# Kernel tuning notes

Measured on AMD Instinct MI355X. Metric: run time of the kernel, lower is better.

Reference implementation:

```python
import jax, jax.numpy as jnp
import numpy as np
from jax import lax

BS, EN, SEQ = 512, 512, 64
D_ENT, D_IN, D_KEY, D_F, H = 256, 1024, 32, 256, 32


def _layer_norm(x, g, b, eps=1e-5):
    m = x.mean(-1, keepdims=True)
    v = ((x - m) ** 2).mean(-1, keepdims=True)
    return (x - m) * lax.rsqrt(v + eps) * g + b


def setup_inputs() -> dict:
    key = jax.random.key(0)
    ks = jax.random.split(key, 24)
    f32 = jnp.float32

    def w(k, shape, fan_in):
        return (jax.random.normal(k, shape, dtype=f32) / np.sqrt(fan_in)).astype(f32)

    inp = {
        'entity_embedding': jax.random.normal(ks[0], (BS, EN, D_ENT), dtype=f32),
        'autoregressive_embedding': jax.random.normal(ks[1], (BS, D_IN), dtype=f32),
        'entity_num': jax.random.randint(ks[2], (BS,), 0, EN),
        'selected_units': jax.random.randint(ks[3], (BS, SEQ), 0, EN),
        'selected_units_num': jax.random.randint(ks[4], (BS,), 0, SEQ),
        # fc_block params (Linear: y = x @ W + b)
        'key_fc_w': w(ks[5], (D_ENT, D_KEY), D_ENT), 'key_fc_b': jnp.zeros((D_KEY,), f32),
        'q1_w': w(ks[6], (D_IN, D_F), D_IN), 'q1_b': jnp.zeros((D_F,), f32),
        'q2_w': w(ks[7], (D_F, D_KEY), D_F), 'q2_b': jnp.zeros((D_KEY,), f32),
        'e1_w': w(ks[8], (D_KEY, D_F), D_KEY), 'e1_b': jnp.zeros((D_F,), f32),
        'e2_w': w(ks[9], (D_F, D_IN), D_F), 'e2_b': jnp.zeros((D_IN,), f32),
        'end_embedding': jax.random.uniform(ks[10], (D_KEY,), dtype=f32,
                                            minval=-1.0 / np.sqrt(D_KEY), maxval=1.0 / np.sqrt(D_KEY)),
        # LayerNorm-LSTM (single layer), gate order: i, f, g, o
        'w_ih': w(ks[11], (D_KEY, 4 * H), D_KEY),
        'w_hh': w(ks[12], (H, 4 * H), H),
        'ln_ig': 1.0 + 0.1 * jax.random.normal(ks[13], (4 * H,), dtype=f32),
        'ln_ib': 0.1 * jax.random.normal(ks[14], (4 * H,), dtype=f32),
        'ln_hg': 1.0 + 0.1 * jax.random.normal(ks[15], (4 * H,), dtype=f32),
        'ln_hb': 0.1 * jax.random.normal(ks[16], (4 * H,), dtype=f32),
        'ln_cg': 1.0 + 0.1 * jax.random.normal(ks[17], (H,), dtype=f32),
        'ln_cb': 0.1 * jax.random.normal(ks[18], (H,), dtype=f32),
    }
    return inp


def _forward(entity_embedding, autoregressive_embedding, entity_num, selected_units,
             selected_units_num, key_fc_w, key_fc_b, q1_w, q1_b, q2_w, q2_b,
             e1_w, e1_b, e2_w, e2_b, end_embedding,
             w_ih, w_hh, ln_ig, ln_ib, ln_hg, ln_hb, ln_cg, ln_cb):
    bs = entity_embedding.shape[0]
    ar = jnp.arange(bs)
    # _get_key_mask: keys for all entities + zero pad slot, end_embedding at slot entity_num
    key = entity_embedding @ key_fc_w + key_fc_b                      # [bs, EN, Dk]
    key = jnp.concatenate([key, jnp.zeros((bs, 1, key.shape[-1]), key.dtype)], axis=1)  # [bs, EN+1, Dk]
    key = key.at[ar, entity_num].set(end_embedding.astype(key.dtype))
    key_embeddings = key                                              # reduce_type == 'selected_units_num'
    base_mask = jnp.arange(key.shape[1])[None, :] < (entity_num + 1)[:, None]  # sequence_mask(entity_num+1)
    mask0 = base_mask.at[ar, entity_num].set(False)                   # end token masked at step 0
    su_prev = jnp.concatenate([selected_units[:, :1], selected_units[:, :-1]], axis=1)

    def step(carry, xs):
        mask, ae, end_flag, one_hot, h, c = carry
        i, su_i, su_p = xs
        # teacher-forced mask evolution
        m1 = jnp.where(i == 1, mask.at[ar, entity_num].set(True), mask)
        m2 = m1.at[ar, su_p].set(False)
        mask = jnp.where(i > 0, m2, mask)
        # query_fc2(query_fc1(ae)) -> LN-LSTM cell
        x = jnp.maximum(ae @ q1_w + q1_b, 0.0) @ q2_w + q2_b
        gates = _layer_norm(x @ w_ih, ln_ig, ln_ib) + _layer_norm(h @ w_hh, ln_hg, ln_hb)
        ig, fg, cg, og = jnp.split(gates, 4, axis=-1)
        c = _layer_norm(jax.nn.sigmoid(fg) * c + jax.nn.sigmoid(ig) * jnp.tanh(cg), ln_cg, ln_cb)
        h = jax.nn.sigmoid(og) * jnp.tanh(c)
        # one-hot scatter of selected unit (skipped once end token seen)
        end_flag = end_flag | (su_i == entity_num)
        one_hot = one_hot.at[ar, su_i].max((~end_flag).astype(one_hot.dtype))
        # mean-pooled embedding of selected units -> embed_fc -> new ae
        emb = jnp.einsum('bn,bnd->bd', one_hot, key_embeddings)
        cnt = one_hot.sum(-1)
        denom = jnp.where((selected_units_num != 0) & (cnt > 0), cnt, 1.0)
        emb = emb / denom[:, None]
        ae = autoregressive_embedding + (jnp.maximum(emb @ e1_w + e1_b, 0.0) @ e2_w + e2_b)
        return (mask, ae, end_flag, one_hot, h, c), (h, mask)

    carry0 = (mask0, autoregressive_embedding,
              jnp.zeros((bs,), bool), jnp.zeros((bs, key.shape[1]), key.dtype),
              jnp.zeros((bs, w_hh.shape[0]), key.dtype), jnp.zeros((bs, w_hh.shape[0]), key.dtype))
    xs = (jnp.arange(selected_units.shape[1]), selected_units.T, su_prev.T)
    _, (queries, masks) = lax.scan(step, carry0, xs)   # [S,bs,Dk], [S,bs,EN+1]
    logits = jnp.einsum('sbd,bnd->sbn', queries, key)
    logits = jnp.where(masks, logits, jnp.asarray(-1e9, logits.dtype))
    return logits.transpose(1, 0, 2)                   # [bs, S, EN+1]


def reference(entity_embedding, autoregressive_embedding, entity_num, selected_units,
              selected_units_num, key_fc_w, key_fc_b, q1_w, q1_b, q2_w, q2_b,
              e1_w, e1_b, e2_w, e2_b, end_embedding,
              w_ih, w_hh, ln_ig, ln_ib, ln_hg, ln_hb, ln_cg, ln_cb):
    return _forward(entity_embedding, autoregressive_embedding, entity_num, selected_units,
                    selected_units_num, key_fc_w, key_fc_b, q1_w, q1_b, q2_w, q2_b,
                    e1_w, e1_b, e2_w, e2_b, end_embedding,
                    w_ih, w_hh, ln_ig, ln_ib, ln_hg, ln_hb, ln_cg, ln_cb)
```

## Files before the change

### kernel.cpp

```cpp
#include <hip/hip_runtime.h>
#include <cstdint>
#include <cstddef>


typedef short bf16x8 __attribute__((ext_vector_type(8)));
typedef float f32x4  __attribute__((ext_vector_type(4)));

__device__ __forceinline__ unsigned f2bf2(float lo, float hi) {
    unsigned r;
    asm("v_cvt_pk_bf16_f32 %0, %1, %2" : "=v"(r) : "v"(lo), "v"(hi));
    return r;
}
__device__ __forceinline__ ushort f2bf(float f) {
    unsigned r;
    asm("v_cvt_pk_bf16_f32 %0, %1, %1" : "=v"(r) : "v"(f));
    return (ushort)r;
}

__device__ __forceinline__ void gld16(const void* g, void* l) {
    __builtin_amdgcn_global_load_lds(
        (const __attribute__((address_space(1))) void*)g,
        (__attribute__((address_space(3))) void*)l,
        16, 0, 0);
}

template<int BM, int BN, int BK, int WR, int WC,
         bool RELU, bool ADDVEC, bool OUT_BF16, bool A_F32, bool KEYMODE>
__global__ __launch_bounds__(WR * WC * 64)
void mfma_gemm(const void* __restrict__ Av, int lda,
               const ushort* __restrict__ BT,
               const float* __restrict__ bias,
               const float* __restrict__ addvec, int ldadd,
               void* __restrict__ outv, int ldo,
               int K, int out_row_offset)
{
    constexpr int NT  = WR * WC * 64;
    constexpr int WM  = BM / WR, WN = BN / WC;
    constexpr int TMt = WM / 16, TNt = WN / 16;
    constexpr int KC  = BK / 8;
    constexpr int CHA = BM * KC, CHB = BN * KC;
    __shared__ __align__(16) ushort As[BM * BK];
    __shared__ __align__(16) ushort Bs[BN * BK];

    const int tid  = threadIdx.x;
    const int lane = tid & 63;
    const int w    = tid >> 6;
    const int wr   = w / WC, wc = w % WC;
    const int row0 = blockIdx.x * BM;
    const int n0   = blockIdx.y * BN;

    f32x4 acc[TMt][TNt];
#pragma unroll
    for (int i = 0; i < TMt; i++)
#pragma unroll
        for (int j = 0; j < TNt; j++)
#pragma unroll
            for (int r = 0; r < 4; r++) acc[i][j][r] = 0.f;

    const ushort* Ab = (const ushort*)Av;
    const float*  Af = (const float*)Av;

    for (int k0 = 0; k0 < K; k0 += BK) {
        if (A_F32) {
#pragma unroll
            for (int id = tid; id < CHA; id += NT) {
                int r = id / KC, kc = id % KC;
                const float* src = Af + (size_t)(row0 + r) * lda + k0 + kc * 8;
                float4 v0 = *(const float4*)(src);
                float4 v1 = *(const float4*)(src + 4);
                uint4 p;
                p.x = f2bf2(v0.x, v0.y);
                p.y = f2bf2(v0.z, v0.w);
                p.z = f2bf2(v1.x, v1.y);
                p.w = f2bf2(v1.z, v1.w);
                *(uint4*)(&As[id * 8]) = p;
            }
        } else {
#pragma unroll
            for (int id = tid; id < CHA; id += NT) {
                int r = id / KC, kc = id % KC;
                gld16(Ab + (size_t)(row0 + r) * lda + k0 + kc * 8, &As[id * 8]);
            }
        }
#pragma unroll
        for (int id = tid; id < CHB; id += NT) {
            int r = id / KC, kc = id % KC;
            gld16(BT + (size_t)(n0 + r) * K + k0 + kc * 8, &Bs[id * 8]);
        }
        __syncthreads();

        bf16x8 afr[TMt], bfr[TNt];
        const int krd = (lane >> 4) * 8;
        const int mrd = lane & 15;
#pragma unroll
        for (int tm = 0; tm < TMt; tm++)
            afr[tm] = *(bf16x8*)(&As[(wr * WM + tm * 16 + mrd) * BK + krd]);
#pragma unroll
        for (int tn = 0; tn < TNt; tn++)
            bfr[tn] = *(bf16x8*)(&Bs[(wc * WN + tn * 16 + mrd) * BK + krd]);
#pragma unroll
        for (int tm = 0; tm < TMt; tm++)
#pragma unroll
            for (int tn = 0; tn < TNt; tn++)
                acc[tm][tn] = __builtin_amdgcn_mfma_f32_16x16x32_bf16(
                    afr[tm], bfr[tn], acc[tm][tn], 0, 0, 0);
        __syncthreads();
    }

    float*  outf = (float*)outv;
    ushort* outh = (ushort*)outv;
    const int cn = lane & 15;
    const int rb = (lane >> 4) * 4;
#pragma unroll
    for (int tm = 0; tm < TMt; tm++) {
#pragma unroll
        for (int r = 0; r < 4; r++) {
            int grow = row0 + wr * WM + tm * 16 + rb + r;
            int b_   = grow & 511;
#pragma unroll
            for (int tn = 0; tn < TNt; tn++) {
                int gcol = n0 + wc * WN + tn * 16 + cn;
                float v = acc[tm][tn][r] + bias[gcol];
                if (RELU)   v = fmaxf(v, 0.f);
                if (ADDVEC) v += addvec[(size_t)b_ * ldadd + gcol];
                size_t oidx;
                if (KEYMODE) oidx = ((size_t)(grow >> 9) * 513 + b_) * 32 + gcol;
                else         oidx = (size_t)(grow + out_row_offset) * ldo + gcol;
                if (OUT_BF16) outh[oidx] = f2bf(v);
                else          outf[oidx] = v;
            }
        }
    }
}

__global__ __launch_bounds__(256) void misc_prep(
    const float* __restrict__ kw,  const float* __restrict__ e1w,
    const float* __restrict__ e2w, const float* __restrict__ q1w,
    const float* __restrict__ q2w,
    ushort* __restrict__ kwt,  ushort* __restrict__ e1wt,
    ushort* __restrict__ e2wt, ushort* __restrict__ q1wt,
    ushort* __restrict__ q2wt,
    const float* __restrict__ ar, ushort* __restrict__ AEb)
{
    int bx = blockIdx.x;
    if (bx < 512) {
        int i = (bx * 256 + threadIdx.x) * 4;
        float4 v = *(const float4*)(ar + i);
        uint2 o;
        o.x = f2bf2(v.x, v.y);
        o.y = f2bf2(v.z, v.w);
        *(uint2*)(AEb + i) = o;
        return;
    }
    bx -= 512;
    const float* W; ushort* WT; int K, N, t0;
    if      (bx < 8)   { W = kw;  WT = kwt;  K = 256;  N = 32;   t0 = bx; }
    else if (bx < 16)  { W = e1w; WT = e1wt; K = 32;   N = 256;  t0 = bx - 8; }
    else if (bx < 272) { W = e2w; WT = e2wt; K = 256;  N = 1024; t0 = bx - 16; }
    else if (bx < 528) { W = q1w; WT = q1wt; K = 1024; N = 256;  t0 = bx - 272; }
    else               { W = q2w; WT = q2wt; K = 256;  N = 32;   t0 = bx - 528; }
    int nn = N >> 5;
    int kt = (t0 / nn) * 32, nt = (t0 % nn) * 32;
    __shared__ float t[32][33];
    int x = threadIdx.x & 31, y = threadIdx.x >> 5;
    for (int i = y; i < 32; i += 8) t[i][x] = W[(size_t)(kt + i) * N + nt + x];
    __syncthreads();
    for (int i = y; i < 32; i += 8) WT[(size_t)(nt + i) * K + kt + x] = f2bf(t[x][i]);
}

__global__ __launch_bounds__(64) void prep_kernel(
    const int* __restrict__ en_g, const int* __restrict__ su_g,
    const int* __restrict__ sun_g, float* __restrict__ key,
    const float* __restrict__ eemb,
    int* __restrict__ fs_g, ushort* __restrict__ EMB)
{
    int b = blockIdx.x;
    int tid = threadIdx.x;
    __shared__ int fs_l[513];
    __shared__ int su_l[64];
    __shared__ float krows[64 * 32];
    for (int i = tid; i < 513; i += 64) fs_l[i] = 64;
    su_l[tid] = su_g[b * 64 + tid];
    int en = en_g[b];
    if (tid < 32) key[((size_t)b * 513 + 512) * 32 + tid] = 0.f;
    else          key[((size_t)b * 513 + en) * 32 + (tid - 32)] = eemb[tid - 32];
    __syncthreads();
    atomicMin(&fs_l[su_l[tid]], tid);
    unsigned long long ball = __ballot(su_l[tid] == en);
    int T = ball ? (__ffsll(ball) - 1) : 64;
    __syncthreads();
    {
        int d = tid & 31;
#pragma unroll 4
        for (int i = 0; i < 32; i++) {
            int r = 2 * i + (tid >> 5);
            krows[r * 32 + d] = key[((size_t)b * 513 + su_l[r]) * 32 + d];
        }
    }
    for (int i = tid; i < 513; i += 64) fs_g[(size_t)b * 513 + i] = fs_l[i];
    __syncthreads();

    int sun = sun_g[b];
    float a = 0.f;
    int cnt = 0;
    for (int i = 0; i < 64; i++) {
        bool nw = (i < T) && (fs_l[su_l[i]] == i);
        if (nw) {
            cnt++;
            if (tid < 32) a += krows[i * 32 + tid];
        }
        float denom = (sun != 0 && cnt > 0) ? (float)cnt : 1.0f;
        if (tid < 32) EMB[((size_t)i * 512 + b) * 32 + tid] = f2bf(a / denom);
    }
}

__device__ inline float sigm(float x) { return 1.0f / (1.0f + expf(-x)); }

__global__ __launch_bounds__(128) void lstm_kernel(
    const float* __restrict__ X, const float* __restrict__ wih_g,
    const float* __restrict__ whh_g,
    const float* __restrict__ lnig, const float* __restrict__ lnib,
    const float* __restrict__ lnhg, const float* __restrict__ lnhb,
    const float* __restrict__ lncg, const float* __restrict__ lncb,
    float* __restrict__ Q)
{
    const int wv = threadIdx.x >> 6;
    const int lane = threadIdx.x & 63;
    const int b = blockIdx.x * 2 + wv;
    __shared__ float xs[2][64 * 32];

    {
        int d = lane & 31;
#pragma unroll 8
        for (int i = 0; i < 32; i++) {
            int s = 2 * i + (lane >> 5);
            xs[wv][s * 32 + d] = X[((size_t)s * 512 + b) * 32 + d];
        }
    }
    float w0[32], w1[32], u0[32], u1[32];
#pragma unroll
    for (int k = 0; k < 32; k++) {
        w0[k] = wih_g[k * 128 + lane];
        w1[k] = wih_g[k * 128 + lane + 64];
        u0[k] = whh_g[k * 128 + lane];
        u1[k] = whh_g[k * 128 + lane + 64];
    }
    const float gi0 = lnig[lane], gi1 = lnig[lane + 64];
    const float bi0 = lnib[lane], bi1 = lnib[lane + 64];
    const float gh0 = lnhg[lane], gh1 = lnhg[lane + 64];
    const float bh0 = lnhb[lane], bh1 = lnhb[lane + 64];
    const int j = lane & 31;
    const float gc = lncg[j], bc = lncb[j];
    float h = 0.f, c = 0.f;
    __syncthreads();

    const float* xrow = &xs[wv][0];
    for (int s = 0; s < 64; s++) {
        float ax0 = 0.f, ax1 = 0.f, ah0 = 0.f, ah1 = 0.f;
#pragma unroll
        for (int k = 0; k < 32; k++) {
            float xk = xrow[s * 32 + k];
            float hk = __shfl(h, k);
            ax0 += xk * w0[k]; ax1 += xk * w1[k];
            ah0 += hk * u0[k]; ah1 += hk * u1[k];
        }
        float r0 = ax0 + ax1, r1 = ax0 * ax0 + ax1 * ax1;
        float r2 = ah0 + ah1, r3 = ah0 * ah0 + ah1 * ah1;
#pragma unroll
        for (int m = 1; m <= 32; m <<= 1) {
            r0 += __shfl_xor(r0, m); r1 += __shfl_xor(r1, m);
            r2 += __shfl_xor(r2, m); r3 += __shfl_xor(r3, m);
        }
        float mx = r0 * (1.f / 128.f), vx = r1 * (1.f / 128.f) - mx * mx;
        float mh = r2 * (1.f / 128.f), vh = r3 * (1.f / 128.f) - mh * mh;
        float sx = rsqrtf(vx + 1e-5f), sh = rsqrtf(vh + 1e-5f);
        float g0 = (ax0 - mx) * sx * gi0 + bi0 + (ah0 - mh) * sh * gh0 + bh0;
        float g1 = (ax1 - mx) * sx * gi1 + bi1 + (ah1 - mh) * sh * gh1 + bh1;
        float igv = __shfl(g0, j),      fgv = __shfl(g0, j + 32);
        float cgv = __shfl(g1, j),      ogv = __shfl(g1, j + 32);
        float cc = sigm(fgv) * c + sigm(igv) * tanhf(cgv);
        float s0 = cc, s1 = cc * cc;
#pragma unroll
        for (int m = 1; m <= 32; m <<= 1) {
            s0 += __shfl_xor(s0, m); s1 += __shfl_xor(s1, m);
        }
        float mc = s0 * (1.f / 64.f), vc = s1 * (1.f / 64.f) - mc * mc;
        c = (cc - mc) * rsqrtf(vc + 1e-5f) * gc + bc;
        h = sigm(ogv) * tanhf(c);
        if (lane < 32) Q[((size_t)b * 64 + s) * 32 + lane] = h;
    }
}

__global__ __launch_bounds__(128) void logits_kernel(
    const float* __restrict__ key, const float* __restrict__ Q,
    const int* __restrict__ fs_g, const int* __restrict__ en_g,
    float* __restrict__ out)
{
    int b = blockIdx.x;
    int n0 = blockIdx.y * 128;
    int tid = threadIdx.x;
    __shared__ float Qs[64 * 32];
    __shared__ float Ks[128 * 33];
    for (int i = tid * 4; i < 2048; i += 512)
        *(float4*)(&Qs[i]) = *(const float4*)(Q + (size_t)b * 2048 + i);
    for (int i = tid; i < 4096; i += 128) {
        int r = i >> 5, d = i & 31;
        int n = n0 + r;
        Ks[r * 33 + d] = (n < 513) ? key[((size_t)b * 513 + n) * 32 + d] : 0.f;
    }
    __syncthreads();
    int n = n0 + tid;
    if (n < 513) {
        int en = en_g[b];
        int f = fs_g[(size_t)b * 513 + n];
        float kreg[32];
#pragma unroll
        for (int d = 0; d < 32; d++) kreg[d] = Ks[tid * 33 + d];
        for (int s = 0; s < 64; s++) {
            float a = 0.f;
#pragma unroll
            for (int d = 0; d < 32; d++) a += Qs[s * 32 + d] * kreg[d];
            bool m = (s == 0) ? (n < en) : ((n <= en) && (f >= s));
            out[((size_t)b * 64 + s) * 513 + n] = m ? a : -1e9f;
        }
    }
}

extern "C" void kernel_launch(void* const* d_in, const int* in_sizes, int n_in,
                              void* d_out, int out_size, void* d_ws, size_t ws_size,
                              hipStream_t stream)
{
    const float* ee   = (const float*)d_in[0];
    const float* ar   = (const float*)d_in[1];
    const int*   en   = (const int*)d_in[2];
    const int*   su   = (const int*)d_in[3];
    const int*   sun  = (const int*)d_in[4];
    const float* kw   = (const float*)d_in[5];
    const float* kb   = (const float*)d_in[6];
    const float* q1w  = (const float*)d_in[7];
    const float* q1b  = (const float*)d_in[8];
    const float* q2w  = (const float*)d_in[9];
    const float* q2b  = (const float*)d_in[10];
    const float* e1w  = (const float*)d_in[11];
    const float* e1b  = (const float*)d_in[12];
    const float* e2w  = (const float*)d_in[13];
    const float* e2b  = (const float*)d_in[14];
    const float* eemb = (const float*)d_in[15];
    const float* wih  = (const float*)d_in[16];
    const float* whh  = (const float*)d_in[17];
    const float* lnig = (const float*)d_in[18];
    const float* lnib = (const float*)d_in[19];
    const float* lnhg = (const float*)d_in[20];
    const float* lnhb = (const float*)d_in[21];
    const float* lncg = (const float*)d_in[22];
    const float* lncb = (const float*)d_in[23];
    float* outp = (float*)d_out;

    char* p = (char*)d_ws;
    float*  key  = (float*)p;  p += (size_t)512 * 513 * 32 * 4;
    ushort* AEb  = (ushort*)p; p += (size_t)32768 * 1024 * 2;
    ushort* Z1b  = (ushort*)p; p += (size_t)32768 * 256 * 2;
    ushort* EMBb = (ushort*)p; p += (size_t)32768 * 32 * 2;
    float*  X    = (float*)p;  p += (size_t)32768 * 32 * 4;
    float*  Q    = (float*)p;  p += (size_t)32768 * 32 * 4;
    int*    fs   = (int*)p;    p += (size_t)512 * 513 * 4;
    ushort* kwt  = (ushort*)p; p += (size_t)32 * 256 * 2;
    ushort* e1wt = (ushort*)p; p += (size_t)256 * 32 * 2;
    ushort* e2wt = (ushort*)p; p += (size_t)1024 * 256 * 2;
    ushort* q1wt = (ushort*)p; p += (size_t)256 * 1024 * 2;
    ushort* q2wt = (ushort*)p; p += (size_t)32 * 256 * 2;

    misc_prep<<<1048, 256, 0, stream>>>(kw, e1w, e2w, q1w, q2w,
                                        kwt, e1wt, e2wt, q1wt, q2wt, ar, AEb);

    mfma_gemm<128, 32, 32, 4, 1, false, false, false, true, true>
        <<<dim3(2048, 1), 256, 0, stream>>>(ee, 256, kwt, kb, nullptr, 0, key, 32, 256, 0);
    prep_kernel<<<512, 64, 0, stream>>>(en, su, sun, key, eemb, fs, EMBb);

    mfma_gemm<128, 128, 32, 2, 2, true, false, true, false, false>
        <<<dim3(252, 2), 256, 0, stream>>>(EMBb, 32, e1wt, e1b, nullptr, 0, Z1b, 256, 32, 0);
    mfma_gemm<128, 128, 32, 2, 2, false, true, true, false, false>
        <<<dim3(252, 8), 256, 0, stream>>>(Z1b, 256, e2wt, e2b, ar, 1024, AEb, 1024, 256, 512);
    mfma_gemm<128, 128, 32, 2, 2, true, false, true, false, false>
        <<<dim3(256, 2), 256, 0, stream>>>(AEb, 1024, q1wt, q1b, nullptr, 0, Z1b, 256, 1024, 0);
    mfma_gemm<128, 32, 32, 4, 1, false, false, false, false, false>
        <<<dim3(256, 1), 256, 0, stream>>>(Z1b, 256, q2wt, q2b, nullptr, 0, X, 32, 256, 0);

    lstm_kernel<<<256, 128, 0, stream>>>(X, wih, whh, lnig, lnib, lnhg, lnhb, lncg, lncb, Q);

    logits_kernel<<<dim3(512, 5), 128, 0, stream>>>(key, Q, fs, en, outp);
}
```

Measured before the change: 699.0 us.

## Fold e2 and q1 linear layers into one precomposed weight, swizzle LDS tiles

Removes the 1024-wide intermediate AE by precomputing W2 = e2_w @ q1_w and a combined bias c2 = e2_b @ q1_w. The q1 pre-activation then comes from a 256-K GEMM plus a per-batch term P0 = ar @ q1_w + q1_b, replacing two large GEMMs and the 32768x1024 bf16 buffer. It also XOR-swizzles the LDS tile layout in the GEMM to avoid bank conflicts, raises BK to 64 for several GEMMs, and vectorizes the Q reads in the logits dot product. Precomposing the weights changes bf16 rounding order, which may shift numerics slightly.

```diff
diff --git a/kernel.cpp b/kernel.cpp
--- a/kernel.cpp
+++ b/kernel.cpp
@@ -38,6 +38,7 @@
     constexpr int WM  = BM / WR, WN = BN / WC;
     constexpr int TMt = WM / 16, TNt = WN / 16;
     constexpr int KC  = BK / 8;
+    constexpr int SWZ = KC - 1;
     constexpr int CHA = BM * KC, CHB = BN * KC;
     __shared__ __align__(16) ushort As[BM * BK];
     __shared__ __align__(16) ushort Bs[BN * BK];
@@ -65,7 +66,8 @@
 #pragma unroll
             for (int id = tid; id < CHA; id += NT) {
                 int r = id / KC, kc = id % KC;
-                const float* src = Af + (size_t)(row0 + r) * lda + k0 + kc * 8;
+                int kcs = kc ^ (r & SWZ);
+                const float* src = Af + (size_t)(row0 + r) * lda + k0 + kcs * 8;
                 float4 v0 = *(const float4*)(src);
                 float4 v1 = *(const float4*)(src + 4);
                 uint4 p;
@@ -79,31 +81,42 @@
 #pragma unroll
             for (int id = tid; id < CHA; id += NT) {
                 int r = id / KC, kc = id % KC;
-                gld16(Ab + (size_t)(row0 + r) * lda + k0 + kc * 8, &As[id * 8]);
+                int kcs = kc ^ (r & SWZ);
+                gld16(Ab + (size_t)(row0 + r) * lda + k0 + kcs * 8, &As[id * 8]);
             }
         }
 #pragma unroll
         for (int id = tid; id < CHB; id += NT) {
             int r = id / KC, kc = id % KC;
-            gld16(BT + (size_t)(n0 + r) * K + k0 + kc * 8, &Bs[id * 8]);
+            int kcs = kc ^ (r & SWZ);
+            gld16(BT + (size_t)(n0 + r) * K + k0 + kcs * 8, &Bs[id * 8]);
         }
         __syncthreads();
 
-        bf16x8 afr[TMt], bfr[TNt];
-        const int krd = (lane >> 4) * 8;
-        const int mrd = lane & 15;
-#pragma unroll
-        for (int tm = 0; tm < TMt; tm++)
-            afr[tm] = *(bf16x8*)(&As[(wr * WM + tm * 16 + mrd) * BK + krd]);
-#pragma unroll
-        for (int tn = 0; tn < TNt; tn++)
-            bfr[tn] = *(bf16x8*)(&Bs[(wc * WN + tn * 16 + mrd) * BK + krd]);
-#pragma unroll
-        for (int tm = 0; tm < TMt; tm++)
-#pragma unroll
-            for (int tn = 0; tn < TNt; tn++)
-                acc[tm][tn] = __builtin_amdgcn_mfma_f32_16x16x32_bf16(
-                    afr[tm], bfr[tn], acc[tm][tn], 0, 0, 0);
+        const int m16 = lane & 15;
+        const int hi  = lane >> 4;
+#pragma unroll
+        for (int kk = 0; kk < BK / 32; kk++) {
+            bf16x8 afr[TMt], bfr[TNt];
+#pragma unroll
+            for (int tm = 0; tm < TMt; tm++) {
+                int row = wr * WM + tm * 16 + m16;
+                int cc  = kk * 4 + hi;
+                afr[tm] = *(bf16x8*)(&As[row * BK + ((cc ^ (row & SWZ)) << 3)]);
+            }
+#pragma unroll
+            for (int tn = 0; tn < TNt; tn++) {
+                int row = wc * WN + tn * 16 + m16;
+                int cc  = kk * 4 + hi;
+                bfr[tn] = *(bf16x8*)(&Bs[row * BK + ((cc ^ (row & SWZ)) << 3)]);
+            }
+#pragma unroll
+            for (int tm = 0; tm < TMt; tm++)
+#pragma unroll
+                for (int tn = 0; tn < TNt; tn++)
+                    acc[tm][tn] = __builtin_amdgcn_mfma_f32_16x16x32_bf16(
+                        afr[tm], bfr[tn], acc[tm][tn], 0, 0, 0);
+        }
         __syncthreads();
     }
 
@@ -121,8 +134,8 @@
             for (int tn = 0; tn < TNt; tn++) {
                 int gcol = n0 + wc * WN + tn * 16 + cn;
                 float v = acc[tm][tn][r] + bias[gcol];
+                if (ADDVEC) v += addvec[(size_t)b_ * ldadd + gcol];
                 if (RELU)   v = fmaxf(v, 0.f);
-                if (ADDVEC) v += addvec[(size_t)b_ * ldadd + gcol];
                 size_t oidx;
                 if (KEYMODE) oidx = ((size_t)(grow >> 9) * 513 + b_) * 32 + gcol;
                 else         oidx = (size_t)(grow + out_row_offset) * ldo + gcol;
@@ -136,29 +149,40 @@
 __global__ __launch_bounds__(256) void misc_prep(
     const float* __restrict__ kw,  const float* __restrict__ e1w,
     const float* __restrict__ e2w, const float* __restrict__ q1w,
-    const float* __restrict__ q2w,
+    const float* __restrict__ q2w, const float* __restrict__ e2b,
     ushort* __restrict__ kwt,  ushort* __restrict__ e1wt,
-    ushort* __restrict__ e2wt, ushort* __restrict__ q1wt,
+    ushort* __restrict__ e2wb, ushort* __restrict__ q1wt,
     ushort* __restrict__ q2wt,
-    const float* __restrict__ ar, ushort* __restrict__ AEb)
+    float* __restrict__ zeros, float* __restrict__ c2)
 {
     int bx = blockIdx.x;
-    if (bx < 512) {
+    if (bx < 256) {
         int i = (bx * 256 + threadIdx.x) * 4;
-        float4 v = *(const float4*)(ar + i);
+        float4 v = *(const float4*)(e2w + i);
         uint2 o;
         o.x = f2bf2(v.x, v.y);
         o.y = f2bf2(v.z, v.w);
-        *(uint2*)(AEb + i) = o;
+        *(uint2*)(e2wb + i) = o;
         return;
     }
-    bx -= 512;
+    if (bx == 256) {
+        zeros[threadIdx.x] = 0.f;
+        return;
+    }
+    if (bx == 537) {
+        int j = threadIdx.x;
+        float acc = 0.f;
+#pragma unroll 16
+        for (int k = 0; k < 1024; k++) acc += e2b[k] * q1w[k * 256 + j];
+        c2[j] = acc;
+        return;
+    }
+    int bx2 = bx - 257;
     const float* W; ushort* WT; int K, N, t0;
-    if      (bx < 8)   { W = kw;  WT = kwt;  K = 256;  N = 32;   t0 = bx; }
-    else if (bx < 16)  { W = e1w; WT = e1wt; K = 32;   N = 256;  t0 = bx - 8; }
-    else if (bx < 272) { W = e2w; WT = e2wt; K = 256;  N = 1024; t0 = bx - 16; }
-    else if (bx < 528) { W = q1w; WT = q1wt; K = 1024; N = 256;  t0 = bx - 272; }
-    else               { W = q2w; WT = q2wt; K = 256;  N = 32;   t0 = bx - 528; }
+    if      (bx2 < 8)   { W = kw;  WT = kwt;  K = 256;  N = 32;   t0 = bx2; }
+    else if (bx2 < 16)  { W = e1w; WT = e1wt; K = 32;   N = 256;  t0 = bx2 - 8; }
+    else if (bx2 < 272) { W = q1w; WT = q1wt; K = 1024; N = 256;  t0 = bx2 - 16; }
+    else                { W = q2w; WT = q2wt; K = 256;  N = 32;   t0 = bx2 - 272; }
     int nn = N >> 5;
     int kt = (t0 / nn) * 32, nt = (t0 % nn) * 32;
     __shared__ float t[32][33];
@@ -166,6 +190,20 @@
     for (int i = y; i < 32; i += 8) t[i][x] = W[(size_t)(kt + i) * N + nt + x];
     __syncthreads();
     for (int i = y; i < 32; i += 8) WT[(size_t)(nt + i) * K + kt + x] = f2bf(t[x][i]);
+}
+
+__global__ __launch_bounds__(256) void relu_y0(
+    const float* __restrict__ P0, ushort* __restrict__ Y1)
+{
+    int i = (blockIdx.x * 256 + threadIdx.x) * 8;
+    float4 a = *(const float4*)(P0 + i);
+    float4 b = *(const float4*)(P0 + i + 4);
+    uint4 o;
+    o.x = f2bf2(fmaxf(a.x, 0.f), fmaxf(a.y, 0.f));
+    o.y = f2bf2(fmaxf(a.z, 0.f), fmaxf(a.w, 0.f));
+    o.z = f2bf2(fmaxf(b.x, 0.f), fmaxf(b.y, 0.f));
+    o.w = f2bf2(fmaxf(b.z, 0.f), fmaxf(b.w, 0.f));
+    *(uint4*)(Y1 + i) = o;
 }
 
 __global__ __launch_bounds__(64) void prep_kernel(
@@ -319,7 +357,11 @@
         for (int s = 0; s < 64; s++) {
             float a = 0.f;
 #pragma unroll
-            for (int d = 0; d < 32; d++) a += Qs[s * 32 + d] * kreg[d];
+            for (int d4 = 0; d4 < 8; d4++) {
+                f32x4 qv = *(const f32x4*)(&Qs[s * 32 + d4 * 4]);
+                a += qv[0] * kreg[d4 * 4 + 0] + qv[1] * kreg[d4 * 4 + 1]
+                   + qv[2] * kreg[d4 * 4 + 2] + qv[3] * kreg[d4 * 4 + 3];
+            }
             bool m = (s == 0) ? (n < en) : ((n <= en) && (f >= s));
             out[((size_t)b * 64 + s) * 513 + n] = m ? a : -1e9f;
         }
@@ -358,33 +400,46 @@
 
     char* p = (char*)d_ws;
     float*  key  = (float*)p;  p += (size_t)512 * 513 * 32 * 4;
-    ushort* AEb  = (ushort*)p; p += (size_t)32768 * 1024 * 2;
-    ushort* Z1b  = (ushort*)p; p += (size_t)32768 * 256 * 2;
-    ushort* EMBb = (ushort*)p; p += (size_t)32768 * 32 * 2;
     float*  X    = (float*)p;  p += (size_t)32768 * 32 * 4;
     float*  Q    = (float*)p;  p += (size_t)32768 * 32 * 4;
+    float*  P0   = (float*)p;  p += (size_t)512 * 256 * 4;
+    float*  c2   = (float*)p;  p += 256 * 4;
+    float*  zeros= (float*)p;  p += 256 * 4;
     int*    fs   = (int*)p;    p += (size_t)512 * 513 * 4;
+    ushort* Z1b  = (ushort*)p; p += (size_t)32768 * 256 * 2;
+    ushort* Y1b  = (ushort*)p; p += (size_t)32768 * 256 * 2;
+    ushort* EMBb = (ushort*)p; p += (size_t)32768 * 32 * 2;
+    ushort* W2t  = (ushort*)p; p += (size_t)256 * 256 * 2;
     ushort* kwt  = (ushort*)p; p += (size_t)32 * 256 * 2;
     ushort* e1wt = (ushort*)p; p += (size_t)256 * 32 * 2;
-    ushort* e2wt = (ushort*)p; p += (size_t)1024 * 256 * 2;
+    ushort* e2wb = (ushort*)p; p += (size_t)256 * 1024 * 2;
     ushort* q1wt = (ushort*)p; p += (size_t)256 * 1024 * 2;
     ushort* q2wt = (ushort*)p; p += (size_t)32 * 256 * 2;
 
-    misc_prep<<<1048, 256, 0, stream>>>(kw, e1w, e2w, q1w, q2w,
-                                        kwt, e1wt, e2wt, q1wt, q2wt, ar, AEb);
-
-    mfma_gemm<128, 32, 32, 4, 1, false, false, false, true, true>
+    misc_prep<<<538, 256, 0, stream>>>(kw, e1w, e2w, q1w, q2w, e2b,
+                                       kwt, e1wt, e2wb, q1wt, q2wt, zeros, c2);
+
+    mfma_gemm<128, 32, 64, 4, 1, false, false, false, true, true>
         <<<dim3(2048, 1), 256, 0, stream>>>(ee, 256, kwt, kb, nullptr, 0, key, 32, 256, 0);
+
+    mfma_gemm<128, 128, 64, 2, 2, false, false, false, true, false>
+        <<<dim3(4, 2), 256, 0, stream>>>(ar, 1024, q1wt, q1b, nullptr, 0, P0, 256, 1024, 0);
+
+    mfma_gemm<128, 128, 64, 2, 2, false, false, true, false, false>
+        <<<dim3(2, 2), 256, 0, stream>>>(q1wt, 1024, e2wb, zeros, nullptr, 0, W2t, 256, 1024, 0);
+
+    relu_y0<<<64, 256, 0, stream>>>(P0, Y1b);
+
     prep_kernel<<<512, 64, 0, stream>>>(en, su, sun, key, eemb, fs, EMBb);
 
     mfma_gemm<128, 128, 32, 2, 2, true, false, true, false, false>
         <<<dim3(252, 2), 256, 0, stream>>>(EMBb, 32, e1wt, e1b, nullptr, 0, Z1b, 256, 32, 0);
-    mfma_gemm<128, 128, 32, 2, 2, false, true, true, false, false>
-        <<<dim3(252, 8), 256, 0, stream>>>(Z1b, 256, e2wt, e2b, ar, 1024, AEb, 1024, 256, 512);
-    mfma_gemm<128, 128, 32, 2, 2, true, false, true, false, false>
-        <<<dim3(256, 2), 256, 0, stream>>>(AEb, 1024, q1wt, q1b, nullptr, 0, Z1b, 256, 1024, 0);
-    mfma_gemm<128, 32, 32, 4, 1, false, false, false, false, false>
-        <<<dim3(256, 1), 256, 0, stream>>>(Z1b, 256, q2wt, q2b, nullptr, 0, X, 32, 256, 0);
+
+    mfma_gemm<128, 128, 64, 2, 2, true, true, true, false, false>
+        <<<dim3(252, 2), 256, 0, stream>>>(Z1b, 256, W2t, c2, P0, 256, Y1b, 256, 256, 512);
+
+    mfma_gemm<128, 32, 64, 4, 1, false, false, false, false, false>
+        <<<dim3(256, 1), 256, 0, stream>>>(Y1b, 256, q2wt, q2b, nullptr, 0, X, 32, 256, 0);
 
     lstm_kernel<<<256, 128, 0, stream>>>(X, wih, whh, lnig, lnib, lnhg, lnhb, lncg, lncb, Q);
 
```

Measured after the change: 719.7 us. +3.0%, slower.
